# Kernel tuning notes

Hardware: AMD Instinct MI355X
Metric: run time of the kernel (lower is better)

Reference implementation:

```python
import jax, jax.numpy as jnp
import numpy as np


def setup_inputs() -> dict:
    key = jax.random.key(0)
    k1, k2 = jax.random.split(key)
    N, K, E = 65536, 8, 64  # tokens, top_k, num_experts
    top_scores = jax.random.normal(k1, (N, K), dtype=jnp.float32)
    selected_experts_indices = jax.random.randint(k2, (N, K), 0, E, dtype=jnp.int32)
    return {
        "top_scores": top_scores,
        "selected_experts_indices": selected_experts_indices,
        "num_experts": E,
        "top_k": K,
    }


def reference(top_scores, selected_experts_indices, num_experts, top_k):
    # Flatten (token, slot) assignments: total = N * top_k
    expert_flat = selected_experts_indices.reshape(-1)

    # Histogram: number of assignments per expert (float32, matching torch impl)
    num_tokens_per_expert = jax.ops.segment_sum(
        jnp.ones_like(expert_flat, dtype=jnp.float32),
        expert_flat,
        num_segments=num_experts,
    )

    # Stable sort by expert id == counting sort: for each output slot, which
    # flattened assignment index lands there. Identical to the torch
    # scatter/cumsum counting-sort since both are stable.
    token_indices_experts_sorted = jnp.argsort(expert_flat, stable=True)

    # Gather routing scores into expert-sorted order
    top_scores_experts_sorted = top_scores.reshape(-1)[token_indices_experts_sorted]

    # Map flattened assignment index back to token index
    token_indices_experts_sorted = token_indices_experts_sorted // top_k

    return (top_scores_experts_sorted, token_indices_experts_sorted, num_tokens_per_expert)
```

## Files before the change

kernel.cpp:

```cpp
#include <hip/hip_runtime.h>

#define TOTAL   524288
#define NEXP    64
#define TOPK    8
#define GSIZE   256
#define BLOCK   1024
#define NWAVE   16
#define CHUNK   (TOTAL / GSIZE)
#define WCHUNK  (CHUNK / NWAVE)
#define ROWSPW  (GSIZE / NWAVE)

__device__ __forceinline__ unsigned long long expert_mask(
        const unsigned long long bb[6], int x) {
    unsigned long long m = ~0ULL;
#pragma unroll
    for (int bit = 0; bit < 6; bit++)
        m &= ((x >> bit) & 1) ? bb[bit] : ~bb[bit];
    return m;
}

__global__ __launch_bounds__(BLOCK) void hist_kernel(const int* __restrict__ idx,
                                                     int* __restrict__ counts) {
    __shared__ int hist[NWAVE][NEXP];
    const int tid = threadIdx.x, lane = tid & 63, wave = tid >> 6;

    const int2 e2 = ((const int2*)idx)[blockIdx.x * (CHUNK / 2) + tid];

    unsigned long long bb0[6], bb1[6];
#pragma unroll
    for (int bit = 0; bit < 6; bit++) {
        bb0[bit] = __ballot((e2.x >> bit) & 1);
        bb1[bit] = __ballot((e2.y >> bit) & 1);
    }
    hist[wave][lane] = __popcll(expert_mask(bb0, lane)) +
                       __popcll(expert_mask(bb1, lane));
    __syncthreads();
    if (tid < NEXP) {
        int s = 0;
#pragma unroll
        for (int w = 0; w < NWAVE; w++) s += hist[w][tid];
        counts[blockIdx.x * NEXP + tid] = s;
    }
}

__global__ __launch_bounds__(BLOCK) void scatter_kernel(
        const float* __restrict__ scores,
        const int*   __restrict__ idx,
        const int*   __restrict__ counts,
        float*       __restrict__ out_scores,
        float*       __restrict__ out_tok,
        float*       __restrict__ out_cnt) {
    __shared__ int part_pre[NWAVE][NEXP];
    __shared__ int part_tot[NWAVE][NEXP];
    __shared__ int wtot[NWAVE][NEXP];
    __shared__ int exscan_pre[NEXP];

    const int tid = threadIdx.x, lane = tid & 63, wave = tid >> 6, b = blockIdx.x;
    const unsigned long long lt  = (1ULL << lane) - 1ULL;
    const unsigned long long own = 1ULL << lane;

    const int2   e2 = ((const int2*)idx)[b * (CHUNK / 2) + tid];
    const float2 s2 = ((const float2*)scores)[b * (CHUNK / 2) + tid];

    int pre = 0, tot = 0;
    {
        const int r0 = wave * ROWSPW;
#pragma unroll
        for (int q = 0; q < ROWSPW; q++) {
            const int bb = r0 + q;
            const int c  = counts[bb * NEXP + lane];
            tot += c;
            pre += (bb < b) ? c : 0;
        }
    }
    part_pre[wave][lane] = pre;
    part_tot[wave][lane] = tot;

    const int e0 = e2.x, e1 = e2.y;
    unsigned long long bb0[6], bb1[6];
#pragma unroll
    for (int bit = 0; bit < 6; bit++) {
        bb0[bit] = __ballot((e0 >> bit) & 1);
        bb1[bit] = __ballot((e1 >> bit) & 1);
    }
    const unsigned long long M0 = expert_mask(bb0, lane);
    const unsigned long long M1 = expert_mask(bb1, lane);
    wtot[wave][lane] = __popcll(M0) + __popcll(M1);
    __syncthreads();

    if (wave == 0) {
        int p = 0, t = 0;
#pragma unroll
        for (int w = 0; w < NWAVE; w++) {
            p += part_pre[w][lane];
            t += part_tot[w][lane];
        }
        if (b == 0) out_cnt[lane] = (float)t;
        int inc = t;
#pragma unroll
        for (int d = 1; d < 64; d <<= 1) {
            const int v = __shfl_up(inc, d, 64);
            if (lane >= d) inc += v;
        }
        exscan_pre[lane] = (inc - t) + p;
    }
    __syncthreads();

    int base = exscan_pre[lane];
#pragma unroll
    for (int w = 0; w < NWAVE; w++)
        base += (w < wave) ? wtot[w][lane] : 0;

    const unsigned long long own0 = __shfl(M0, e0, 64);
    const unsigned long long own1 = __shfl(M1, e1, 64);
    const unsigned long long c01  = __shfl(M1, e0, 64);
    const unsigned long long c10  = __shfl(M0, e1, 64);
    const int base0 = __shfl(base, e0, 64);
    const int base1 = __shfl(base, e1, 64);

    const int rank0 = __popcll(own0 & lt) + __popcll(c01 & lt);
    const int rank1 = __popcll(c10 & (lt | own)) + __popcll(own1 & lt);

    const int f0 = b * CHUNK + 2 * tid;
    const int pos0 = base0 + rank0;
    const int pos1 = base1 + rank1;

    out_scores[pos0] = s2.x;
    out_scores[pos1] = s2.y;
    out_tok[pos0]    = (float)(f0 >> 3);
    out_tok[pos1]    = (float)((f0 + 1) >> 3);
}

extern "C" void kernel_launch(void* const* d_in, const int* in_sizes, int n_in,
                              void* d_out, int out_size, void* d_ws, size_t ws_size,
                              hipStream_t stream) {
    const float* top_scores = (const float*)d_in[0];
    const int*   sel_idx    = (const int*)d_in[1];
    float*       out        = (float*)d_out;
    int*         counts     = (int*)d_ws;

    float* out_scores = out;
    float* out_tok    = out + TOTAL;
    float* out_cnt    = out + 2 * TOTAL;

    hist_kernel<<<GSIZE, BLOCK, 0, stream>>>(sel_idx, counts);
    scatter_kernel<<<GSIZE, BLOCK, 0, stream>>>(top_scores, sel_idx, counts,
                                                out_scores, out_tok, out_cnt);
}
```

Measured before the change: 67.43 us.

## Fuse histogram and scatter kernels into one cooperative launch with grid sync

Merges the per-block histogram kernel and the scatter kernel into a single cooperative kernel that uses a grid-wide sync between phases. Each block keeps its expert masks and loaded indices and scores in registers across the sync, so the index array is read once and one kernel launch disappears. In exchange it adds a grid barrier and depends on all 256 blocks of 1024 threads being co-resident, which cooperative launch requires.

```diff
diff --git a/kernel.cpp b/kernel.cpp
--- a/kernel.cpp
+++ b/kernel.cpp
@@ -1,4 +1,7 @@
 #include <hip/hip_runtime.h>
+#include <hip/hip_cooperative_groups.h>
+
+namespace cg = cooperative_groups;
 
 #define TOTAL   524288
 #define NEXP    64
@@ -7,7 +10,6 @@
 #define BLOCK   1024
 #define NWAVE   16
 #define CHUNK   (TOTAL / GSIZE)
-#define WCHUNK  (CHUNK / NWAVE)
 #define ROWSPW  (GSIZE / NWAVE)
 
 __device__ __forceinline__ unsigned long long expert_mask(
@@ -19,40 +21,16 @@
     return m;
 }
 
-__global__ __launch_bounds__(BLOCK) void hist_kernel(const int* __restrict__ idx,
-                                                     int* __restrict__ counts) {
-    __shared__ int hist[NWAVE][NEXP];
-    const int tid = threadIdx.x, lane = tid & 63, wave = tid >> 6;
-
-    const int2 e2 = ((const int2*)idx)[blockIdx.x * (CHUNK / 2) + tid];
-
-    unsigned long long bb0[6], bb1[6];
-#pragma unroll
-    for (int bit = 0; bit < 6; bit++) {
-        bb0[bit] = __ballot((e2.x >> bit) & 1);
-        bb1[bit] = __ballot((e2.y >> bit) & 1);
-    }
-    hist[wave][lane] = __popcll(expert_mask(bb0, lane)) +
-                       __popcll(expert_mask(bb1, lane));
-    __syncthreads();
-    if (tid < NEXP) {
-        int s = 0;
-#pragma unroll
-        for (int w = 0; w < NWAVE; w++) s += hist[w][tid];
-        counts[blockIdx.x * NEXP + tid] = s;
-    }
-}
-
-__global__ __launch_bounds__(BLOCK) void scatter_kernel(
+__global__ __launch_bounds__(BLOCK) void fused_kernel(
         const float* __restrict__ scores,
         const int*   __restrict__ idx,
-        const int*   __restrict__ counts,
+        int*         __restrict__ counts,
         float*       __restrict__ out_scores,
         float*       __restrict__ out_tok,
         float*       __restrict__ out_cnt) {
+    __shared__ int wtot[NWAVE][NEXP];
     __shared__ int part_pre[NWAVE][NEXP];
     __shared__ int part_tot[NWAVE][NEXP];
-    __shared__ int wtot[NWAVE][NEXP];
     __shared__ int exscan_pre[NEXP];
 
     const int tid = threadIdx.x, lane = tid & 63, wave = tid >> 6, b = blockIdx.x;
@@ -61,6 +39,27 @@
 
     const int2   e2 = ((const int2*)idx)[b * (CHUNK / 2) + tid];
     const float2 s2 = ((const float2*)scores)[b * (CHUNK / 2) + tid];
+
+    const int e0 = e2.x, e1 = e2.y;
+    unsigned long long bb0[6], bb1[6];
+#pragma unroll
+    for (int bit = 0; bit < 6; bit++) {
+        bb0[bit] = __ballot((e0 >> bit) & 1);
+        bb1[bit] = __ballot((e1 >> bit) & 1);
+    }
+    const unsigned long long M0 = expert_mask(bb0, lane);
+    const unsigned long long M1 = expert_mask(bb1, lane);
+    wtot[wave][lane] = __popcll(M0) + __popcll(M1);
+    __syncthreads();
+
+    if (wave == 0) {
+        int t = 0;
+#pragma unroll
+        for (int w = 0; w < NWAVE; w++) t += wtot[w][lane];
+        counts[b * NEXP + lane] = t;
+    }
+
+    cg::this_grid().sync();
 
     int pre = 0, tot = 0;
     {
@@ -75,17 +74,6 @@
     }
     part_pre[wave][lane] = pre;
     part_tot[wave][lane] = tot;
-
-    const int e0 = e2.x, e1 = e2.y;
-    unsigned long long bb0[6], bb1[6];
-#pragma unroll
-    for (int bit = 0; bit < 6; bit++) {
-        bb0[bit] = __ballot((e0 >> bit) & 1);
-        bb1[bit] = __ballot((e1 >> bit) & 1);
-    }
-    const unsigned long long M0 = expert_mask(bb0, lane);
-    const unsigned long long M1 = expert_mask(bb1, lane);
-    wtot[wave][lane] = __popcll(M0) + __popcll(M1);
     __syncthreads();
 
     if (wave == 0) {
@@ -121,7 +109,7 @@
     const int rank0 = __popcll(own0 & lt) + __popcll(c01 & lt);
     const int rank1 = __popcll(c10 & (lt | own)) + __popcll(own1 & lt);
 
-    const int f0 = b * CHUNK + 2 * tid;
+    const int f0   = b * CHUNK + 2 * tid;
     const int pos0 = base0 + rank0;
     const int pos1 = base1 + rank1;
 
@@ -143,7 +131,8 @@
     float* out_tok    = out + TOTAL;
     float* out_cnt    = out + 2 * TOTAL;
 
-    hist_kernel<<<GSIZE, BLOCK, 0, stream>>>(sel_idx, counts);
-    scatter_kernel<<<GSIZE, BLOCK, 0, stream>>>(top_scores, sel_idx, counts,
-                                                out_scores, out_tok, out_cnt);
+    void* args[] = {(void*)&top_scores, (void*)&sel_idx, (void*)&counts,
+                    (void*)&out_scores, (void*)&out_tok, (void*)&out_cnt};
+    hipLaunchCooperativeKernel((void*)fused_kernel, dim3(GSIZE), dim3(BLOCK),
+                               args, 0, stream);
 }
```

New measurement: 98.45 us. 1.46x slower.

## Stage scatter through LDS in expert-sorted order for coalesced global writes

Applied to the files above, without the earlier changes.

Each block first computes a block-local expert-sorted position for its elements and writes scores, token ids and global positions into shared memory. After a barrier, threads read the staged data in local sorted order and write to global memory, so consecutive threads hit mostly contiguous addresses within each expert segment. This replaces fully random global scatter writes with more coalesced ones, at the cost of 24KB extra LDS, an additional block barrier and a per-wave local scan.

```diff
diff --git a/kernel.cpp b/kernel.cpp
--- a/kernel.cpp
+++ b/kernel.cpp
@@ -7,7 +7,6 @@
 #define BLOCK   1024
 #define NWAVE   16
 #define CHUNK   (TOTAL / GSIZE)
-#define WCHUNK  (CHUNK / NWAVE)
 #define ROWSPW  (GSIZE / NWAVE)
 
 __device__ __forceinline__ unsigned long long expert_mask(
@@ -50,10 +49,13 @@
         float*       __restrict__ out_scores,
         float*       __restrict__ out_tok,
         float*       __restrict__ out_cnt) {
-    __shared__ int part_pre[NWAVE][NEXP];
-    __shared__ int part_tot[NWAVE][NEXP];
-    __shared__ int wtot[NWAVE][NEXP];
-    __shared__ int exscan_pre[NEXP];
+    __shared__ int   wtot[NWAVE][NEXP];
+    __shared__ int   part_pre[NWAVE][NEXP];
+    __shared__ int   part_tot[NWAVE][NEXP];
+    __shared__ int   exscan_pre[NEXP];
+    __shared__ float sc_s[CHUNK];
+    __shared__ float tk_s[CHUNK];
+    __shared__ int   gp_s[CHUNK];
 
     const int tid = threadIdx.x, lane = tid & 63, wave = tid >> 6, b = blockIdx.x;
     const unsigned long long lt  = (1ULL << lane) - 1ULL;
@@ -88,6 +90,21 @@
     wtot[wave][lane] = __popcll(M0) + __popcll(M1);
     __syncthreads();
 
+    int t_pre_w = 0, t_blk = 0;
+#pragma unroll
+    for (int w = 0; w < NWAVE; w++) {
+        const int c = wtot[w][lane];
+        t_pre_w += (w < wave) ? c : 0;
+        t_blk   += c;
+    }
+    int linc = t_blk;
+#pragma unroll
+    for (int d = 1; d < 64; d <<= 1) {
+        const int v = __shfl_up(linc, d, 64);
+        if (lane >= d) linc += v;
+    }
+    const int base_local = (linc - t_blk) + t_pre_w;
+
     if (wave == 0) {
         int p = 0, t = 0;
 #pragma unroll
@@ -106,29 +123,36 @@
     }
     __syncthreads();
 
-    int base = exscan_pre[lane];
-#pragma unroll
-    for (int w = 0; w < NWAVE; w++)
-        base += (w < wave) ? wtot[w][lane] : 0;
+    const int base_glob = exscan_pre[lane] + t_pre_w;
 
     const unsigned long long own0 = __shfl(M0, e0, 64);
     const unsigned long long own1 = __shfl(M1, e1, 64);
     const unsigned long long c01  = __shfl(M1, e0, 64);
     const unsigned long long c10  = __shfl(M0, e1, 64);
-    const int base0 = __shfl(base, e0, 64);
-    const int base1 = __shfl(base, e1, 64);
+    const int bl0 = __shfl(base_local, e0, 64);
+    const int bl1 = __shfl(base_local, e1, 64);
+    const int bg0 = __shfl(base_glob, e0, 64);
+    const int bg1 = __shfl(base_glob, e1, 64);
 
     const int rank0 = __popcll(own0 & lt) + __popcll(c01 & lt);
     const int rank1 = __popcll(c10 & (lt | own)) + __popcll(own1 & lt);
 
     const int f0 = b * CHUNK + 2 * tid;
-    const int pos0 = base0 + rank0;
-    const int pos1 = base1 + rank1;
+    const int l0 = bl0 + rank0, l1 = bl1 + rank1;
+    const int g0 = bg0 + rank0, g1 = bg1 + rank1;
 
-    out_scores[pos0] = s2.x;
-    out_scores[pos1] = s2.y;
-    out_tok[pos0]    = (float)(f0 >> 3);
-    out_tok[pos1]    = (float)((f0 + 1) >> 3);
+    sc_s[l0] = s2.x;             sc_s[l1] = s2.y;
+    tk_s[l0] = (float)(f0 >> 3); tk_s[l1] = (float)((f0 + 1) >> 3);
+    gp_s[l0] = g0;               gp_s[l1] = g1;
+    __syncthreads();
+
+#pragma unroll
+    for (int r = 0; r < 2; r++) {
+        const int i = tid + r * BLOCK;
+        const int p = gp_s[i];
+        out_scores[p] = sc_s[i];
+        out_tok[p]    = tk_s[i];
+    }
 }
 
 extern "C" void kernel_launch(void* const* d_in, const int* in_sizes, int n_in,
```

After: 66.63 us. No clear change (-1.2%).
